# Kernel optimization log

Hardware: AMD Instinct MI355X
Metric: run time of the kernel (lower is better)

The kernel has to match this reference:

```python
import jax, jax.numpy as jnp
import numpy as np

N_NODES = 50000
EPS = 1e-5


def _gcn_edges(edge_index, num_nodes):
    # Add self loops (PyG GCNConv default) and compute symmetric normalization.
    src = jnp.concatenate([edge_index[0], jnp.arange(num_nodes, dtype=edge_index.dtype)])
    dst = jnp.concatenate([edge_index[1], jnp.arange(num_nodes, dtype=edge_index.dtype)])
    deg = jax.ops.segment_sum(jnp.ones_like(dst, dtype=jnp.float32), dst, num_segments=num_nodes)
    dinv = jnp.where(deg > 0, jax.lax.rsqrt(deg), 0.0)
    norm = dinv[src] * dinv[dst]  # [E+N]
    return src, dst, norm


def gcn_conv(x, W, b, src, dst, norm, num_nodes):
    xw = x @ W  # [N, out]
    msg = xw[src] * norm[:, None]  # [E+N, out] gather + scale
    out = jax.ops.segment_sum(msg, dst, num_segments=num_nodes)  # scatter-add
    return out + b


def layer_norm(x, g, b):
    mu = jnp.mean(x, axis=-1, keepdims=True)
    var = jnp.mean(jnp.square(x - mu), axis=-1, keepdims=True)
    return (x - mu) * jax.lax.rsqrt(var + EPS) * g + b


def setup_inputs() -> dict:
    key = jax.random.key(0)
    ks = jax.random.split(key, 12)
    d_in, d_h, d_out = 128, 128, 64
    n_edges = 800000
    x = jax.random.normal(ks[0], (N_NODES, d_in), dtype=jnp.float32)
    edge_index = jax.random.randint(ks[1], (2, n_edges), 0, N_NODES, dtype=jnp.int64)
    s = 1.0 / np.sqrt(d_in)
    return {
        "x": x,
        "edge_index": edge_index,
        "W1": jax.random.uniform(ks[2], (d_in, d_h), jnp.float32, -s, s),
        "b1": jnp.zeros((d_h,), jnp.float32),
        "W2": jax.random.uniform(ks[3], (d_h, d_h), jnp.float32, -s, s),
        "b2": jnp.zeros((d_h,), jnp.float32),
        "W3": jax.random.uniform(ks[4], (d_h, d_out), jnp.float32, -s, s),
        "b3": jnp.zeros((d_out,), jnp.float32),
        "g1": jnp.ones((d_h,), jnp.float32),
        "be1": jnp.zeros((d_h,), jnp.float32),
        "g2": jnp.ones((d_h,), jnp.float32),
        "be2": jnp.zeros((d_h,), jnp.float32),
    }


def reference(x, edge_index, W1, b1, W2, b2, W3, b3, g1, be1, g2, be2):
    num_nodes = x.shape[0]
    src, dst, norm = _gcn_edges(edge_index, num_nodes)
    h = jax.nn.relu(gcn_conv(x, W1, b1, src, dst, norm, num_nodes))
    h = layer_norm(h, g1, be1)  # dropout is identity in eval mode
    h = jax.nn.relu(gcn_conv(h, W2, b2, src, dst, norm, num_nodes))
    h = layer_norm(h, g2, be2)
    return gcn_conv(h, W3, b3, src, dst, norm, num_nodes)
```

## Files before the change

kernel.cpp:

```cpp
#include <hip/hip_runtime.h>

#define EPSV 1e-5f

typedef _Float16 half2_t __attribute__((ext_vector_type(2)));
typedef _Float16 half8_t __attribute__((ext_vector_type(8)));
typedef float float4_t __attribute__((ext_vector_type(4)));
typedef int int4_t __attribute__((ext_vector_type(4)));

#define BINSH 6
#define BINSZ 64


__global__ __launch_bounds__(256) void k_pre(
    const float* __restrict__ W1, const float* __restrict__ W2,
    const float* __restrict__ W3, _Float16* __restrict__ Wh1,
    _Float16* __restrict__ Wh2, _Float16* __restrict__ Wh3,
    int* __restrict__ cursor, _Float16* __restrict__ ys_y,
    _Float16* __restrict__ ys3, int N, int N1, int zb) {
  int bid = blockIdx.x;
  if (bid < 20) {
    const float* W;
    _Float16* Wh;
    int COLS, t;
    if (bid < 8) { W = W1; Wh = Wh1; COLS = 128; t = bid * 256 + threadIdx.x; }
    else if (bid < 16) { W = W2; Wh = Wh2; COLS = 128; t = (bid - 8) * 256 + threadIdx.x; }
    else { W = W3; Wh = Wh3; COLS = 64; t = (bid - 16) * 256 + threadIdx.x; }
    int NT = (COLS / 16) * 4 * 64;
    if (t >= NT) return;
    int lane = t & 63;
    int ks = (t >> 6) & 3;
    int nb = t >> 8;
    int col = nb * 16 + (lane & 15);
    int k0 = ks * 32 + (lane >> 4) * 8;
    half8_t v;
#pragma unroll
    for (int j = 0; j < 8; j++) v[j] = (_Float16)W[(size_t)(k0 + j) * COLS + col];
    *(half8_t*)&Wh[(size_t)t * 8] = v;
    return;
  }
  if (bid < 20 + zb) {
    int i4 = (bid - 20) * 256 + threadIdx.x;
    if (i4 < ((N1 + 3) >> 2)) {
      int4_t z4 = {0, 0, 0, 0};
      ((int4_t*)cursor)[i4] = z4;
    }
    return;
  }
  int t = threadIdx.x;
  half8_t z;
#pragma unroll
  for (int j = 0; j < 8; j++) z[j] = (_Float16)0.f;
  if (t < 16) {
    int s = t >> 2, qq = t & 3;
    *(half8_t*)&ys_y[((size_t)s * N1 + N) * 32 + qq * 8] = z;
  } else if (t < 24) {
    int j = t - 16;
    int s = j >> 2, qq = j & 3;
    *(half8_t*)&ys3[((size_t)s * N1 + N) * 32 + qq * 8] = z;
  }
}


__global__ __launch_bounds__(256) void k_init(
    const int* __restrict__ src, const int* __restrict__ dst,
    int* __restrict__ cursor, unsigned short* __restrict__ csr, int E, int N) {
  int b = blockIdx.x;
  int slice = b & 7;
  int lo = (int)(((long long)N * slice) >> 3);
  int hi = (int)(((long long)N * (slice + 1)) >> 3);
  int r = (b >> 3) * 256 + threadIdx.x;
  const int stride = (4096 >> 3) * 256;
  int E4 = E >> 2;
  const int4_t* dst4 = (const int4_t*)dst;
  const int4_t* src4 = (const int4_t*)src;
  for (int e4 = r; e4 < E4; e4 += stride) {
    int4_t d4 = dst4[e4];
    int4_t s4 = src4[e4];
#pragma unroll
    for (int j = 0; j < 4; j++) {
      int d = d4[j];
      if (d >= lo && d < hi) {
        int pos = atomicAdd(&cursor[d], 1);
        if (pos < BINSZ) csr[((size_t)d << BINSH) + pos] = (unsigned short)s4[j];
      }
    }
  }
  if ((E & 3) && (b >> 3) == 0) {
    for (int e = (E & ~3) + threadIdx.x; e < E; e += 256) {
      int d = dst[e];
      if (d >= lo && d < hi) {
        int s = src[e];
        int pos = atomicAdd(&cursor[d], 1);
        if (pos < BINSZ) csr[((size_t)d << BINSH) + pos] = (unsigned short)s;
      }
    }
  }
}


template <int COLS, bool LN, bool SCALE, typename AT>
__device__ __forceinline__ void gemm_body(
    int bx, const AT* __restrict__ A, const float2* __restrict__ lnp,
    const float* __restrict__ g, const float* __restrict__ be,
    const _Float16* __restrict__ Wh, const int* __restrict__ cursor,
    _Float16* __restrict__ out, int N, int N1) {
  constexpr int NB = COLS / 16;
  int lane = threadIdx.x & 63;
  int w = threadIdx.x >> 6;
  int quad = lane >> 4;
  int mrow = bx * 64 + w * 16 + (lane & 15);
  half8_t af[4];
  if (mrow < N) {
    if constexpr (LN) {
      float P = 0.f, Q = 0.f;
#pragma unroll
      for (int s = 0; s < 4; s++) {
        float2 pq = lnp[(size_t)s * N + mrow];
        P += pq.x; Q += pq.y;
      }
      float mean = P * (1.f / 128.f);
      float rstd = rsqrtf(Q * (1.f / 128.f) - mean * mean + EPSV);
#pragma unroll
      for (int ks = 0; ks < 4; ks++) {
        half8_t sv = *(const half8_t*)&A[((size_t)ks * N1 + mrow) * 32 + quad * 8];
        float4 g0 = *(const float4*)&g[ks * 32 + quad * 8];
        float4 g1 = *(const float4*)&g[ks * 32 + quad * 8 + 4];
        float4 e0 = *(const float4*)&be[ks * 32 + quad * 8];
        float4 e1 = *(const float4*)&be[ks * 32 + quad * 8 + 4];
        af[ks][0] = (_Float16)fmaf(((float)sv[0] - mean) * rstd, g0.x, e0.x);
        af[ks][1] = (_Float16)fmaf(((float)sv[1] - mean) * rstd, g0.y, e0.y);
        af[ks][2] = (_Float16)fmaf(((float)sv[2] - mean) * rstd, g0.z, e0.z);
        af[ks][3] = (_Float16)fmaf(((float)sv[3] - mean) * rstd, g0.w, e0.w);
        af[ks][4] = (_Float16)fmaf(((float)sv[4] - mean) * rstd, g1.x, e1.x);
        af[ks][5] = (_Float16)fmaf(((float)sv[5] - mean) * rstd, g1.y, e1.y);
        af[ks][6] = (_Float16)fmaf(((float)sv[6] - mean) * rstd, g1.z, e1.z);
        af[ks][7] = (_Float16)fmaf(((float)sv[7] - mean) * rstd, g1.w, e1.w);
      }
    } else {
      const AT* ap = A + (size_t)mrow * 128 + quad * 8;
#pragma unroll
      for (int ks = 0; ks < 4; ks++) {
        float4 f0 = *(const float4*)(ap + ks * 32);
        float4 f1 = *(const float4*)(ap + ks * 32 + 4);
        af[ks][0] = (_Float16)f0.x; af[ks][1] = (_Float16)f0.y;
        af[ks][2] = (_Float16)f0.z; af[ks][3] = (_Float16)f0.w;
        af[ks][4] = (_Float16)f1.x; af[ks][5] = (_Float16)f1.y;
        af[ks][6] = (_Float16)f1.z; af[ks][7] = (_Float16)f1.w;
      }
    }
  } else {
#pragma unroll
    for (int ks = 0; ks < 4; ks++)
#pragma unroll
      for (int j = 0; j < 8; j++) af[ks][j] = (_Float16)0.f;
  }
  float4_t acc[NB];
#pragma unroll
  for (int nb = 0; nb < NB; nb++) acc[nb] = (float4_t){0.f, 0.f, 0.f, 0.f};
#pragma unroll
  for (int nb = 0; nb < NB; nb++) {
#pragma unroll
    for (int ks = 0; ks < 4; ks++) {
      half8_t bf = *(const half8_t*)&Wh[(size_t)((nb * 4 + ks) * 64 + lane) * 8];
      acc[nb] = __builtin_amdgcn_mfma_f32_16x16x32_f16(af[ks], bf, acc[nb], 0, 0, 0);
    }
  }
  int orow0 = bx * 64 + w * 16 + quad * 4;
#pragma unroll
  for (int r = 0; r < 4; r++) {
    int row = orow0 + r;
    if (row < N) {
      float dv = 1.f;
      if constexpr (SCALE) dv = rsqrtf((float)(min(cursor[row], BINSZ) + 1));
#pragma unroll
      for (int nb = 0; nb < NB; nb++) {
        int dim = nb * 16 + (lane & 15);
        out[((size_t)(dim >> 5) * N1 + row) * 32 + (dim & 31)] =
            (_Float16)(acc[nb][r] * dv);
      }
    }
  }
}

template <int COLS, bool LN, bool SCALE, typename AT>
__global__ __launch_bounds__(256) void k_gemm_mfma(
    const AT* __restrict__ A, const float2* __restrict__ lnp,
    const float* __restrict__ g, const float* __restrict__ be,
    const _Float16* __restrict__ Wh, const int* __restrict__ cursor,
    _Float16* __restrict__ out, int N, int N1) {
  gemm_body<COLS, LN, SCALE, AT>(blockIdx.x, A, lnp, g, be, Wh, cursor, out, N, N1);
}


__global__ __launch_bounds__(256) void k_aggs(
    const _Float16* __restrict__ ysrc, const unsigned short* __restrict__ csr,
    const int* __restrict__ cursor, const float* __restrict__ b,
    _Float16* __restrict__ sdst, float2* __restrict__ lnp, int N, int N1) {
  int slice = blockIdx.x & 3;
  int lane = threadIdx.x & 63;
  int g = lane >> 4, li = lane & 15;
  int q = li & 3, es = li >> 2;
  int node = (blockIdx.x >> 2) * 16 + (threadIdx.x >> 6) * 4 + g;
  const half8_t* yb = (const half8_t*)ysrc + (size_t)slice * N1 * 4;
  int cnt = 0;
  if (node < N) cnt = min(cursor[node], BINSZ);
  int cround = (cnt + 15) & ~15;
  size_t bin = (size_t)node << BINSH;
  float acc[8];
#pragma unroll
  for (int j = 0; j < 8; j++) acc[j] = 0.f;
  const half2_t one2 = {(_Float16)1.f, (_Float16)1.f};
  for (int c = 0; c < cround; c += 16) {
    int idx = N;
    if (c + li < cnt) idx = (int)csr[bin + c + li];
#pragma unroll
    for (int p = 0; p < 2; p++) {
      int sa = __shfl(idx, (g << 4) | (es << 2) | (p << 1), 64);
      int sb = __shfl(idx, (g << 4) | (es << 2) | (p << 1) | 1, 64);
      half8_t ua = yb[(size_t)sa * 4 + q];
      half8_t ub = yb[(size_t)sb * 4 + q];
      const unsigned int* wa = (const unsigned int*)&ua;
      const unsigned int* wb = (const unsigned int*)&ub;
#pragma unroll
      for (int w = 0; w < 4; w++) {
        unsigned int p0 = __builtin_amdgcn_perm(wa[w], wb[w], 0x01000504u);
        unsigned int p1 = __builtin_amdgcn_perm(wa[w], wb[w], 0x03020706u);
        acc[2 * w] = __builtin_amdgcn_fdot2(
            __builtin_bit_cast(half2_t, p0), one2, acc[2 * w], false);
        acc[2 * w + 1] = __builtin_amdgcn_fdot2(
            __builtin_bit_cast(half2_t, p1), one2, acc[2 * w + 1], false);
      }
    }
  }
#pragma unroll
  for (int j = 0; j < 8; j++) {
    acc[j] += __shfl_xor(acc[j], 4, 64);
    acc[j] += __shfl_xor(acc[j], 8, 64);
  }
  half8_t us = yb[(size_t)min(node, N) * 4 + q];
#pragma unroll
  for (int j = 0; j < 8; j++) acc[j] += (float)us[j];
  float di = rsqrtf((float)(cnt + 1));
  float4 b0 = ((const float4*)b)[slice * 8 + q * 2];
  float4 b1 = ((const float4*)b)[slice * 8 + q * 2 + 1];
  float v[8];
  v[0] = fmaxf(fmaf(acc[0], di, b0.x), 0.f);
  v[1] = fmaxf(fmaf(acc[1], di, b0.y), 0.f);
  v[2] = fmaxf(fmaf(acc[2], di, b0.z), 0.f);
  v[3] = fmaxf(fmaf(acc[3], di, b0.w), 0.f);
  v[4] = fmaxf(fmaf(acc[4], di, b1.x), 0.f);
  v[5] = fmaxf(fmaf(acc[5], di, b1.y), 0.f);
  v[6] = fmaxf(fmaf(acc[6], di, b1.z), 0.f);
  v[7] = fmaxf(fmaf(acc[7], di, b1.w), 0.f);
  float p = 0.f, qs = 0.f;
#pragma unroll
  for (int j = 0; j < 8; j++) {
    p += v[j];
    qs = fmaf(v[j], v[j], qs);
  }
  p += __shfl_xor(p, 1, 64);
  p += __shfl_xor(p, 2, 64);
  qs += __shfl_xor(qs, 1, 64);
  qs += __shfl_xor(qs, 2, 64);
  if (node < N) {
    if (li == 0) lnp[(size_t)slice * N + node] = make_float2(p, qs);
    if (es == 0) {
      half8_t o;
#pragma unroll
      for (int j = 0; j < 8; j++) o[j] = (_Float16)v[j];
      ((half8_t*)sdst)[((size_t)slice * N1 + node) * 4 + q] = o;
    }
  }
}


__global__ __launch_bounds__(256) void k_agg_out(
    const _Float16* __restrict__ ysrc, const unsigned short* __restrict__ csr,
    const int* __restrict__ cursor, const float* __restrict__ b,
    float* __restrict__ out, int N, int N1) {
  int slice = blockIdx.x & 1;
  int lane = threadIdx.x & 63;
  int g = lane >> 4, li = lane & 15;
  int q = li & 3, es = li >> 2;
  int node = (blockIdx.x >> 1) * 16 + (threadIdx.x >> 6) * 4 + g;
  const half8_t* yb = (const half8_t*)ysrc + (size_t)slice * N1 * 4;
  int cnt = 0;
  if (node < N) cnt = min(cursor[node], BINSZ);
  int cround = (cnt + 15) & ~15;
  size_t bin = (size_t)node << BINSH;
  float acc[8];
#pragma unroll
  for (int j = 0; j < 8; j++) acc[j] = 0.f;
  const half2_t one2 = {(_Float16)1.f, (_Float16)1.f};
  for (int c = 0; c < cround; c += 16) {
    int idx = N;
    if (c + li < cnt) idx = (int)csr[bin + c + li];
#pragma unroll
    for (int p = 0; p < 2; p++) {
      int sa = __shfl(idx, (g << 4) | (es << 2) | (p << 1), 64);
      int sb = __shfl(idx, (g << 4) | (es << 2) | (p << 1) | 1, 64);
      half8_t ua = yb[(size_t)sa * 4 + q];
      half8_t ub = yb[(size_t)sb * 4 + q];
      const unsigned int* wa = (const unsigned int*)&ua;
      const unsigned int* wb = (const unsigned int*)&ub;
#pragma unroll
      for (int w = 0; w < 4; w++) {
        unsigned int p0 = __builtin_amdgcn_perm(wa[w], wb[w], 0x01000504u);
        unsigned int p1 = __builtin_amdgcn_perm(wa[w], wb[w], 0x03020706u);
        acc[2 * w] = __builtin_amdgcn_fdot2(
            __builtin_bit_cast(half2_t, p0), one2, acc[2 * w], false);
        acc[2 * w + 1] = __builtin_amdgcn_fdot2(
            __builtin_bit_cast(half2_t, p1), one2, acc[2 * w + 1], false);
      }
    }
  }
#pragma unroll
  for (int j = 0; j < 8; j++) {
    acc[j] += __shfl_xor(acc[j], 4, 64);
    acc[j] += __shfl_xor(acc[j], 8, 64);
  }
  if (node < N && es == 0) {
    half8_t us = yb[(size_t)node * 4 + q];
#pragma unroll
    for (int j = 0; j < 8; j++) acc[j] += (float)us[j];
    float di = rsqrtf((float)(cnt + 1));
    float4 b0 = ((const float4*)b)[slice * 8 + q * 2];
    float4 b1 = ((const float4*)b)[slice * 8 + q * 2 + 1];
    float4 o0, o1;
    o0.x = fmaf(acc[0], di, b0.x);
    o0.y = fmaf(acc[1], di, b0.y);
    o0.z = fmaf(acc[2], di, b0.z);
    o0.w = fmaf(acc[3], di, b0.w);
    o1.x = fmaf(acc[4], di, b1.x);
    o1.y = fmaf(acc[5], di, b1.y);
    o1.z = fmaf(acc[6], di, b1.z);
    o1.w = fmaf(acc[7], di, b1.w);
    ((float4*)out)[(size_t)node * 16 + slice * 8 + q * 2] = o0;
    ((float4*)out)[(size_t)node * 16 + slice * 8 + q * 2 + 1] = o1;
  }
}


extern "C" void kernel_launch(void* const* d_in, const int* in_sizes, int n_in,
                              void* d_out, int out_size, void* d_ws, size_t ws_size,
                              hipStream_t stream) {
  const float* x = (const float*)d_in[0];
  const int* ei = (const int*)d_in[1];
  const float* W1 = (const float*)d_in[2];
  const float* b1 = (const float*)d_in[3];
  const float* W2 = (const float*)d_in[4];
  const float* b2 = (const float*)d_in[5];
  const float* W3 = (const float*)d_in[6];
  const float* b3 = (const float*)d_in[7];
  const float* g1 = (const float*)d_in[8];
  const float* be1 = (const float*)d_in[9];
  const float* g2 = (const float*)d_in[10];
  const float* be2 = (const float*)d_in[11];

  int N = in_sizes[0] / 128;
  int E = in_sizes[1] / 2;
  int N1 = N + 1;
  const int* srcs = ei;
  const int* dsts = ei + E;

  char* ws = (char*)d_ws;
  size_t off = 0;
  auto alloc = [&](size_t bytes) -> char* {
    char* p = ws + off;
    off = (off + bytes + 255) & ~(size_t)255;
    return p;
  };
  int* cursor = (int*)alloc((size_t)N1 * 4 + 16);
  unsigned short* csr = (unsigned short*)alloc((size_t)N * BINSZ * 2);
  _Float16* ys_y = (_Float16*)alloc((size_t)4 * N1 * 32 * 2);
  _Float16* ys_s = (_Float16*)alloc((size_t)4 * N1 * 32 * 2);
  _Float16* ys3 = (_Float16*)alloc((size_t)2 * N1 * 32 * 2);
  float2* lnp = (float2*)alloc((size_t)4 * N * 8);
  _Float16* Wh1 = (_Float16*)alloc(128 * 128 * 2);
  _Float16* Wh2 = (_Float16*)alloc(128 * 128 * 2);
  _Float16* Wh3 = (_Float16*)alloc(128 * 64 * 2);

  int gb = (N + 63) / 64;
  int nb16 = (N + 15) / 16;
  int zb = (((N1 + 3) >> 2) + 255) >> 8;

  k_pre<<<20 + zb + 1, 256, 0, stream>>>(W1, W2, W3, Wh1, Wh2, Wh3,
                                         cursor, ys_y, ys3, N, N1, zb);
  k_init<<<4096, 256, 0, stream>>>(srcs, dsts, cursor, csr, E, N);
  k_gemm_mfma<128, false, true, float><<<gb, 256, 0, stream>>>(
      x, nullptr, nullptr, nullptr, Wh1, cursor, ys_y, N, N1);
  k_aggs<<<nb16 * 4, 256, 0, stream>>>(ys_y, csr, cursor, b1, ys_s, lnp, N, N1);
  k_gemm_mfma<128, true, true, _Float16><<<gb, 256, 0, stream>>>(
      ys_s, lnp, g1, be1, Wh2, cursor, ys_y, N, N1);
  k_aggs<<<nb16 * 4, 256, 0, stream>>>(ys_y, csr, cursor, b2, ys_s, lnp, N, N1);
  k_gemm_mfma<64, true, true, _Float16><<<gb, 256, 0, stream>>>(
      ys_s, lnp, g2, be2, Wh3, cursor, ys3, N, N1);
  k_agg_out<<<nb16 * 2, 256, 0, stream>>>(ys3, csr, cursor, b3,
                                          (float*)d_out, N, N1);
}
```

Baseline: 246.1 us.

## Fuse aggregation, layernorm and next-layer GEMM into one kernel via LDS

Merges each hidden-layer aggregation kernel with the following LN+GEMM kernel. A 512-thread block aggregates 64 nodes into shared memory along with per-slice LN partial sums, then runs the MFMA GEMM straight from LDS. This removes the global round trip of the intermediate activations and the lnp buffer, plus two launches. The cost is fewer, larger blocks: one per 64 nodes instead of one per 16 nodes per slice, each wave looping over 8 node groups serially, plus a block barrier. That may lower the parallelism available to hide gather latency.

```diff
diff --git a/kernel.cpp b/kernel.cpp
--- a/kernel.cpp
+++ b/kernel.cpp
@@ -15,8 +15,9 @@
     const float* __restrict__ W1, const float* __restrict__ W2,
     const float* __restrict__ W3, _Float16* __restrict__ Wh1,
     _Float16* __restrict__ Wh2, _Float16* __restrict__ Wh3,
-    int* __restrict__ cursor, _Float16* __restrict__ ys_y,
-    _Float16* __restrict__ ys3, int N, int N1, int zb) {
+    int* __restrict__ cursor, _Float16* __restrict__ ys_a,
+    _Float16* __restrict__ ys_b, _Float16* __restrict__ ys3,
+    int N, int N1, int zb) {
   int bid = blockIdx.x;
   if (bid < 20) {
     const float* W;
@@ -52,9 +53,13 @@
   for (int j = 0; j < 8; j++) z[j] = (_Float16)0.f;
   if (t < 16) {
     int s = t >> 2, qq = t & 3;
-    *(half8_t*)&ys_y[((size_t)s * N1 + N) * 32 + qq * 8] = z;
-  } else if (t < 24) {
+    *(half8_t*)&ys_a[((size_t)s * N1 + N) * 32 + qq * 8] = z;
+  } else if (t < 32) {
     int j = t - 16;
+    int s = j >> 2, qq = j & 3;
+    *(half8_t*)&ys_b[((size_t)s * N1 + N) * 32 + qq * 8] = z;
+  } else if (t < 40) {
+    int j = t - 32;
     int s = j >> 2, qq = j & 3;
     *(half8_t*)&ys3[((size_t)s * N1 + N) * 32 + qq * 8] = z;
   }
@@ -98,55 +103,25 @@
 }
 
 
-template <int COLS, bool LN, bool SCALE, typename AT>
-__device__ __forceinline__ void gemm_body(
-    int bx, const AT* __restrict__ A, const float2* __restrict__ lnp,
-    const float* __restrict__ g, const float* __restrict__ be,
-    const _Float16* __restrict__ Wh, const int* __restrict__ cursor,
-    _Float16* __restrict__ out, int N, int N1) {
-  constexpr int NB = COLS / 16;
+__global__ __launch_bounds__(256) void k_gemm1(
+    const float* __restrict__ A, const _Float16* __restrict__ Wh,
+    const int* __restrict__ cursor, _Float16* __restrict__ out, int N, int N1) {
+  constexpr int NB = 8;
   int lane = threadIdx.x & 63;
   int w = threadIdx.x >> 6;
   int quad = lane >> 4;
-  int mrow = bx * 64 + w * 16 + (lane & 15);
+  int mrow = blockIdx.x * 64 + w * 16 + (lane & 15);
   half8_t af[4];
   if (mrow < N) {
-    if constexpr (LN) {
-      float P = 0.f, Q = 0.f;
-#pragma unroll
-      for (int s = 0; s < 4; s++) {
-        float2 pq = lnp[(size_t)s * N + mrow];
-        P += pq.x; Q += pq.y;
-      }
-      float mean = P * (1.f / 128.f);
-      float rstd = rsqrtf(Q * (1.f / 128.f) - mean * mean + EPSV);
-#pragma unroll
-      for (int ks = 0; ks < 4; ks++) {
-        half8_t sv = *(const half8_t*)&A[((size_t)ks * N1 + mrow) * 32 + quad * 8];
-        float4 g0 = *(const float4*)&g[ks * 32 + quad * 8];
-        float4 g1 = *(const float4*)&g[ks * 32 + quad * 8 + 4];
-        float4 e0 = *(const float4*)&be[ks * 32 + quad * 8];
-        float4 e1 = *(const float4*)&be[ks * 32 + quad * 8 + 4];
-        af[ks][0] = (_Float16)fmaf(((float)sv[0] - mean) * rstd, g0.x, e0.x);
-        af[ks][1] = (_Float16)fmaf(((float)sv[1] - mean) * rstd, g0.y, e0.y);
-        af[ks][2] = (_Float16)fmaf(((float)sv[2] - mean) * rstd, g0.z, e0.z);
-        af[ks][3] = (_Float16)fmaf(((float)sv[3] - mean) * rstd, g0.w, e0.w);
-        af[ks][4] = (_Float16)fmaf(((float)sv[4] - mean) * rstd, g1.x, e1.x);
-        af[ks][5] = (_Float16)fmaf(((float)sv[5] - mean) * rstd, g1.y, e1.y);
-        af[ks][6] = (_Float16)fmaf(((float)sv[6] - mean) * rstd, g1.z, e1.z);
-        af[ks][7] = (_Float16)fmaf(((float)sv[7] - mean) * rstd, g1.w, e1.w);
-      }
-    } else {
-      const AT* ap = A + (size_t)mrow * 128 + quad * 8;
-#pragma unroll
-      for (int ks = 0; ks < 4; ks++) {
-        float4 f0 = *(const float4*)(ap + ks * 32);
-        float4 f1 = *(const float4*)(ap + ks * 32 + 4);
-        af[ks][0] = (_Float16)f0.x; af[ks][1] = (_Float16)f0.y;
-        af[ks][2] = (_Float16)f0.z; af[ks][3] = (_Float16)f0.w;
-        af[ks][4] = (_Float16)f1.x; af[ks][5] = (_Float16)f1.y;
-        af[ks][6] = (_Float16)f1.z; af[ks][7] = (_Float16)f1.w;
-      }
+    const float* ap = A + (size_t)mrow * 128 + quad * 8;
+#pragma unroll
+    for (int ks = 0; ks < 4; ks++) {
+      float4 f0 = *(const float4*)(ap + ks * 32);
+      float4 f1 = *(const float4*)(ap + ks * 32 + 4);
+      af[ks][0] = (_Float16)f0.x; af[ks][1] = (_Float16)f0.y;
+      af[ks][2] = (_Float16)f0.z; af[ks][3] = (_Float16)f0.w;
+      af[ks][4] = (_Float16)f1.x; af[ks][5] = (_Float16)f1.y;
+      af[ks][6] = (_Float16)f1.z; af[ks][7] = (_Float16)f1.w;
     }
   } else {
 #pragma unroll
@@ -165,13 +140,12 @@
       acc[nb] = __builtin_amdgcn_mfma_f32_16x16x32_f16(af[ks], bf, acc[nb], 0, 0, 0);
     }
   }
-  int orow0 = bx * 64 + w * 16 + quad * 4;
+  int orow0 = blockIdx.x * 64 + w * 16 + quad * 4;
 #pragma unroll
   for (int r = 0; r < 4; r++) {
     int row = orow0 + r;
     if (row < N) {
-      float dv = 1.f;
-      if constexpr (SCALE) dv = rsqrtf((float)(min(cursor[row], BINSZ) + 1));
+      float dv = rsqrtf((float)(min(cursor[row], BINSZ) + 1));
 #pragma unroll
       for (int nb = 0; nb < NB; nb++) {
         int dim = nb * 16 + (lane & 15);
@@ -182,93 +156,161 @@
   }
 }
 
-template <int COLS, bool LN, bool SCALE, typename AT>
-__global__ __launch_bounds__(256) void k_gemm_mfma(
-    const AT* __restrict__ A, const float2* __restrict__ lnp,
-    const float* __restrict__ g, const float* __restrict__ be,
-    const _Float16* __restrict__ Wh, const int* __restrict__ cursor,
-    _Float16* __restrict__ out, int N, int N1) {
-  gemm_body<COLS, LN, SCALE, AT>(blockIdx.x, A, lnp, g, be, Wh, cursor, out, N, N1);
-}
-
-
-__global__ __launch_bounds__(256) void k_aggs(
+
+template <int COLS>
+__global__ __launch_bounds__(512) void k_agg_gemm(
     const _Float16* __restrict__ ysrc, const unsigned short* __restrict__ csr,
     const int* __restrict__ cursor, const float* __restrict__ b,
-    _Float16* __restrict__ sdst, float2* __restrict__ lnp, int N, int N1) {
-  int slice = blockIdx.x & 3;
-  int lane = threadIdx.x & 63;
-  int g = lane >> 4, li = lane & 15;
+    const float* __restrict__ g, const float* __restrict__ be,
+    const _Float16* __restrict__ Wh, _Float16* __restrict__ out,
+    int N, int N1) {
+  __shared__ _Float16 sA[64][136];
+  __shared__ float2 slnp[64][4];
+  int tid = threadIdx.x;
+  int wave = tid >> 6;
+  int lane = tid & 63;
+  int slice = wave & 3;
+  int half = wave >> 2;
+  int g4 = lane >> 4, li = lane & 15;
   int q = li & 3, es = li >> 2;
-  int node = (blockIdx.x >> 2) * 16 + (threadIdx.x >> 6) * 4 + g;
   const half8_t* yb = (const half8_t*)ysrc + (size_t)slice * N1 * 4;
-  int cnt = 0;
-  if (node < N) cnt = min(cursor[node], BINSZ);
-  int cround = (cnt + 15) & ~15;
-  size_t bin = (size_t)node << BINSH;
-  float acc[8];
-#pragma unroll
-  for (int j = 0; j < 8; j++) acc[j] = 0.f;
   const half2_t one2 = {(_Float16)1.f, (_Float16)1.f};
-  for (int c = 0; c < cround; c += 16) {
-    int idx = N;
-    if (c + li < cnt) idx = (int)csr[bin + c + li];
-#pragma unroll
-    for (int p = 0; p < 2; p++) {
-      int sa = __shfl(idx, (g << 4) | (es << 2) | (p << 1), 64);
-      int sb = __shfl(idx, (g << 4) | (es << 2) | (p << 1) | 1, 64);
-      half8_t ua = yb[(size_t)sa * 4 + q];
-      half8_t ub = yb[(size_t)sb * 4 + q];
-      const unsigned int* wa = (const unsigned int*)&ua;
-      const unsigned int* wb = (const unsigned int*)&ub;
-#pragma unroll
-      for (int w = 0; w < 4; w++) {
-        unsigned int p0 = __builtin_amdgcn_perm(wa[w], wb[w], 0x01000504u);
-        unsigned int p1 = __builtin_amdgcn_perm(wa[w], wb[w], 0x03020706u);
-        acc[2 * w] = __builtin_amdgcn_fdot2(
-            __builtin_bit_cast(half2_t, p0), one2, acc[2 * w], false);
-        acc[2 * w + 1] = __builtin_amdgcn_fdot2(
-            __builtin_bit_cast(half2_t, p1), one2, acc[2 * w + 1], false);
-      }
-    }
-  }
-#pragma unroll
-  for (int j = 0; j < 8; j++) {
-    acc[j] += __shfl_xor(acc[j], 4, 64);
-    acc[j] += __shfl_xor(acc[j], 8, 64);
-  }
-  half8_t us = yb[(size_t)min(node, N) * 4 + q];
-#pragma unroll
-  for (int j = 0; j < 8; j++) acc[j] += (float)us[j];
-  float di = rsqrtf((float)(cnt + 1));
-  float4 b0 = ((const float4*)b)[slice * 8 + q * 2];
-  float4 b1 = ((const float4*)b)[slice * 8 + q * 2 + 1];
-  float v[8];
-  v[0] = fmaxf(fmaf(acc[0], di, b0.x), 0.f);
-  v[1] = fmaxf(fmaf(acc[1], di, b0.y), 0.f);
-  v[2] = fmaxf(fmaf(acc[2], di, b0.z), 0.f);
-  v[3] = fmaxf(fmaf(acc[3], di, b0.w), 0.f);
-  v[4] = fmaxf(fmaf(acc[4], di, b1.x), 0.f);
-  v[5] = fmaxf(fmaf(acc[5], di, b1.y), 0.f);
-  v[6] = fmaxf(fmaf(acc[6], di, b1.z), 0.f);
-  v[7] = fmaxf(fmaf(acc[7], di, b1.w), 0.f);
-  float p = 0.f, qs = 0.f;
-#pragma unroll
-  for (int j = 0; j < 8; j++) {
-    p += v[j];
-    qs = fmaf(v[j], v[j], qs);
-  }
-  p += __shfl_xor(p, 1, 64);
-  p += __shfl_xor(p, 2, 64);
-  qs += __shfl_xor(qs, 1, 64);
-  qs += __shfl_xor(qs, 2, 64);
-  if (node < N) {
-    if (li == 0) lnp[(size_t)slice * N + node] = make_float2(p, qs);
-    if (es == 0) {
-      half8_t o;
-#pragma unroll
-      for (int j = 0; j < 8; j++) o[j] = (_Float16)v[j];
-      ((half8_t*)sdst)[((size_t)slice * N1 + node) * 4 + q] = o;
+  for (int t = 0; t < 8; t++) {
+    int rloc = half * 32 + t * 4 + g4;
+    int node = blockIdx.x * 64 + rloc;
+    int cnt = 0;
+    if (node < N) cnt = min(cursor[node], BINSZ);
+    int cround = (cnt + 15) & ~15;
+    size_t bin = (size_t)node << BINSH;
+    float acc[8];
+#pragma unroll
+    for (int j = 0; j < 8; j++) acc[j] = 0.f;
+    for (int c = 0; c < cround; c += 16) {
+      int idx = N;
+      if (c + li < cnt) idx = (int)csr[bin + c + li];
+#pragma unroll
+      for (int p = 0; p < 2; p++) {
+        int sa = __shfl(idx, (g4 << 4) | (es << 2) | (p << 1), 64);
+        int sb = __shfl(idx, (g4 << 4) | (es << 2) | (p << 1) | 1, 64);
+        half8_t ua = yb[(size_t)sa * 4 + q];
+        half8_t ub = yb[(size_t)sb * 4 + q];
+        const unsigned int* wa = (const unsigned int*)&ua;
+        const unsigned int* wb = (const unsigned int*)&ub;
+#pragma unroll
+        for (int w = 0; w < 4; w++) {
+          unsigned int p0 = __builtin_amdgcn_perm(wa[w], wb[w], 0x01000504u);
+          unsigned int p1 = __builtin_amdgcn_perm(wa[w], wb[w], 0x03020706u);
+          acc[2 * w] = __builtin_amdgcn_fdot2(
+              __builtin_bit_cast(half2_t, p0), one2, acc[2 * w], false);
+          acc[2 * w + 1] = __builtin_amdgcn_fdot2(
+              __builtin_bit_cast(half2_t, p1), one2, acc[2 * w + 1], false);
+        }
+      }
+    }
+#pragma unroll
+    for (int j = 0; j < 8; j++) {
+      acc[j] += __shfl_xor(acc[j], 4, 64);
+      acc[j] += __shfl_xor(acc[j], 8, 64);
+    }
+    half8_t us = yb[(size_t)min(node, N) * 4 + q];
+#pragma unroll
+    for (int j = 0; j < 8; j++) acc[j] += (float)us[j];
+    float di = rsqrtf((float)(cnt + 1));
+    float4 b0 = ((const float4*)b)[slice * 8 + q * 2];
+    float4 b1 = ((const float4*)b)[slice * 8 + q * 2 + 1];
+    float v[8];
+    v[0] = fmaxf(fmaf(acc[0], di, b0.x), 0.f);
+    v[1] = fmaxf(fmaf(acc[1], di, b0.y), 0.f);
+    v[2] = fmaxf(fmaf(acc[2], di, b0.z), 0.f);
+    v[3] = fmaxf(fmaf(acc[3], di, b0.w), 0.f);
+    v[4] = fmaxf(fmaf(acc[4], di, b1.x), 0.f);
+    v[5] = fmaxf(fmaf(acc[5], di, b1.y), 0.f);
+    v[6] = fmaxf(fmaf(acc[6], di, b1.z), 0.f);
+    v[7] = fmaxf(fmaf(acc[7], di, b1.w), 0.f);
+    float p = 0.f, qs = 0.f;
+#pragma unroll
+    for (int j = 0; j < 8; j++) {
+      p += v[j];
+      qs = fmaf(v[j], v[j], qs);
+    }
+    p += __shfl_xor(p, 1, 64);
+    p += __shfl_xor(p, 2, 64);
+    qs += __shfl_xor(qs, 1, 64);
+    qs += __shfl_xor(qs, 2, 64);
+    if (node < N) {
+      if (li == 0) slnp[rloc][slice] = make_float2(p, qs);
+      if (es == 0) {
+        half8_t o;
+#pragma unroll
+        for (int j = 0; j < 8; j++) o[j] = (_Float16)v[j];
+        *(half8_t*)&sA[rloc][slice * 32 + q * 8] = o;
+      }
+    }
+  }
+  __syncthreads();
+  constexpr int NB = COLS / 16;
+  constexpr int NBH = NB / 2;
+  int rb = wave & 3;
+  int ch = wave >> 2;
+  int quad = lane >> 4;
+  int mloc = rb * 16 + (lane & 15);
+  int mrow = blockIdx.x * 64 + mloc;
+  half8_t af[4];
+  if (mrow < N) {
+    float P = 0.f, Q = 0.f;
+#pragma unroll
+    for (int s = 0; s < 4; s++) {
+      float2 pq = slnp[mloc][s];
+      P += pq.x; Q += pq.y;
+    }
+    float mean = P * (1.f / 128.f);
+    float rstd = rsqrtf(Q * (1.f / 128.f) - mean * mean + EPSV);
+#pragma unroll
+    for (int ks = 0; ks < 4; ks++) {
+      half8_t sv = *(const half8_t*)&sA[mloc][ks * 32 + quad * 8];
+      float4 g0 = *(const float4*)&g[ks * 32 + quad * 8];
+      float4 g1 = *(const float4*)&g[ks * 32 + quad * 8 + 4];
+      float4 e0 = *(const float4*)&be[ks * 32 + quad * 8];
+      float4 e1 = *(const float4*)&be[ks * 32 + quad * 8 + 4];
+      af[ks][0] = (_Float16)fmaf(((float)sv[0] - mean) * rstd, g0.x, e0.x);
+      af[ks][1] = (_Float16)fmaf(((float)sv[1] - mean) * rstd, g0.y, e0.y);
+      af[ks][2] = (_Float16)fmaf(((float)sv[2] - mean) * rstd, g0.z, e0.z);
+      af[ks][3] = (_Float16)fmaf(((float)sv[3] - mean) * rstd, g0.w, e0.w);
+      af[ks][4] = (_Float16)fmaf(((float)sv[4] - mean) * rstd, g1.x, e1.x);
+      af[ks][5] = (_Float16)fmaf(((float)sv[5] - mean) * rstd, g1.y, e1.y);
+      af[ks][6] = (_Float16)fmaf(((float)sv[6] - mean) * rstd, g1.z, e1.z);
+      af[ks][7] = (_Float16)fmaf(((float)sv[7] - mean) * rstd, g1.w, e1.w);
+    }
+  } else {
+#pragma unroll
+    for (int ks = 0; ks < 4; ks++)
+#pragma unroll
+      for (int j = 0; j < 8; j++) af[ks][j] = (_Float16)0.f;
+  }
+  float4_t acc2[NBH];
+#pragma unroll
+  for (int nb = 0; nb < NBH; nb++) acc2[nb] = (float4_t){0.f, 0.f, 0.f, 0.f};
+#pragma unroll
+  for (int nb = 0; nb < NBH; nb++) {
+    int nbg = ch * NBH + nb;
+#pragma unroll
+    for (int ks = 0; ks < 4; ks++) {
+      half8_t bf = *(const half8_t*)&Wh[(size_t)((nbg * 4 + ks) * 64 + lane) * 8];
+      acc2[nb] = __builtin_amdgcn_mfma_f32_16x16x32_f16(af[ks], bf, acc2[nb], 0, 0, 0);
+    }
+  }
+  int orow0 = blockIdx.x * 64 + rb * 16 + quad * 4;
+#pragma unroll
+  for (int r = 0; r < 4; r++) {
+    int row = orow0 + r;
+    if (row < N) {
+      float dv = rsqrtf((float)(min(cursor[row], BINSZ) + 1));
+#pragma unroll
+      for (int nb = 0; nb < NBH; nb++) {
+        int dim = (ch * NBH + nb) * 16 + (lane & 15);
+        out[((size_t)(dim >> 5) * N1 + row) * 32 + (dim & 31)] =
+            (_Float16)(acc2[nb][r] * dv);
+      }
     }
   }
 }
@@ -372,10 +414,9 @@
   };
   int* cursor = (int*)alloc((size_t)N1 * 4 + 16);
   unsigned short* csr = (unsigned short*)alloc((size_t)N * BINSZ * 2);
-  _Float16* ys_y = (_Float16*)alloc((size_t)4 * N1 * 32 * 2);
-  _Float16* ys_s = (_Float16*)alloc((size_t)4 * N1 * 32 * 2);
+  _Float16* ys_a = (_Float16*)alloc((size_t)4 * N1 * 32 * 2);
+  _Float16* ys_b = (_Float16*)alloc((size_t)4 * N1 * 32 * 2);
   _Float16* ys3 = (_Float16*)alloc((size_t)2 * N1 * 32 * 2);
-  float2* lnp = (float2*)alloc((size_t)4 * N * 8);
   _Float16* Wh1 = (_Float16*)alloc(128 * 128 * 2);
   _Float16* Wh2 = (_Float16*)alloc(128 * 128 * 2);
   _Float16* Wh3 = (_Float16*)alloc(128 * 64 * 2);
@@ -385,16 +426,13 @@
   int zb = (((N1 + 3) >> 2) + 255) >> 8;
 
   k_pre<<<20 + zb + 1, 256, 0, stream>>>(W1, W2, W3, Wh1, Wh2, Wh3,
-                                         cursor, ys_y, ys3, N, N1, zb);
+                                         cursor, ys_a, ys_b, ys3, N, N1, zb);
   k_init<<<4096, 256, 0, stream>>>(srcs, dsts, cursor, csr, E, N);
-  k_gemm_mfma<128, false, true, float><<<gb, 256, 0, stream>>>(
-      x, nullptr, nullptr, nullptr, Wh1, cursor, ys_y, N, N1);
-  k_aggs<<<nb16 * 4, 256, 0, stream>>>(ys_y, csr, cursor, b1, ys_s, lnp, N, N1);
-  k_gemm_mfma<128, true, true, _Float16><<<gb, 256, 0, stream>>>(
-      ys_s, lnp, g1, be1, Wh2, cursor, ys_y, N, N1);
-  k_aggs<<<nb16 * 4, 256, 0, stream>>>(ys_y, csr, cursor, b2, ys_s, lnp, N, N1);
-  k_gemm_mfma<64, true, true, _Float16><<<gb, 256, 0, stream>>>(
-      ys_s, lnp, g2, be2, Wh3, cursor, ys3, N, N1);
+  k_gemm1<<<gb, 256, 0, stream>>>(x, Wh1, cursor, ys_a, N, N1);
+  k_agg_gemm<128><<<gb, 512, 0, stream>>>(ys_a, csr, cursor, b1, g1, be1,
+                                          Wh2, ys_b, N, N1);
+  k_agg_gemm<64><<<gb, 512, 0, stream>>>(ys_b, csr, cursor, b2, g2, be2,
+                                         Wh3, ys3, N, N1);
   k_agg_out<<<nb16 * 2, 256, 0, stream>>>(ys3, csr, cursor, b3,
                                           (float*)d_out, N, N1);
 }
```

After: 295.3 us. +20.0%, slower.
